# Optimization experiments

Measured on AMD Instinct MI355X. Metric: run time of the kernel, lower is better.

Reference implementation:

```python
import jax, jax.numpy as jnp
import numpy as np


def setup_inputs() -> dict:
    key = jax.random.key(0)
    ks = jax.random.split(key, 5)
    B, S, D = 2, 2048, 1024
    x = jax.random.normal(ks[0], (B, S, D), dtype=jnp.float32)
    # nn.Linear default init scale ~ 1/sqrt(fan_in); use scaled normals
    W_qkv = jax.random.normal(ks[1], (3 * D, D), dtype=jnp.float32) * (1.0 / np.sqrt(D))
    b_qkv = jax.random.normal(ks[2], (3 * D,), dtype=jnp.float32) * 0.01
    W_out = jax.random.normal(ks[3], (D, D), dtype=jnp.float32) * (1.0 / np.sqrt(D))
    b_out = jax.random.normal(ks[4], (D,), dtype=jnp.float32) * 0.01
    return {"x": x, "W_qkv": W_qkv, "b_qkv": b_qkv, "W_out": W_out, "b_out": b_out, "n_heads": 16}


def reference(x, W_qkv, b_qkv, W_out, b_out, n_heads):
    B, S, D = x.shape
    H = n_heads
    c = D // H
    scale = jnp.asarray(1.0 / np.sqrt(c), dtype=x.dtype)
    # qkv projection; torch layout: (head, qkv, c) along the 3*D output dim
    qkv = (x @ W_qkv.T + b_qkv).reshape(B, S, H, 3, c)
    q = qkv[..., 0, :]  # (B, S, H, c)
    k = qkv[..., 1, :]
    v = qkv[..., 2, :]
    scores = jnp.einsum("bshd,bthd->bhst", q, k) * scale  # (B, H, S, S)
    # mask='right': forbid attending to future positions (col > row)
    causal = jnp.arange(S)[None, :] > jnp.arange(S)[:, None]  # (S, S) True where future
    scores = jnp.where(causal[None, None], -jnp.inf, scores)
    attn = jax.nn.softmax(scores, axis=-1)
    ctx = jnp.einsum("bhst,bthd->bshd", attn, v).reshape(B, S, D)
    return ctx @ W_out.T + b_out
```

## Files before the change

### kernel.cpp

```cpp
#include <hip/hip_runtime.h>
#include <stdint.h>

#define B_ 2
#define S_ 2048
#define D_ 1024
#define H_ 16
#define C_ 64
#define M_ (B_*S_)
#define N1_ (3*D_)

typedef float f32x4 __attribute__((ext_vector_type(4)));
typedef float f32x16 __attribute__((ext_vector_type(16)));
typedef __bf16 bf16x8 __attribute__((ext_vector_type(8)));

#define QSCALE 0.18033688f

static __device__ __forceinline__ unsigned short f2bf(float f) {
  __bf16 h = (__bf16)f;
  return __builtin_bit_cast(unsigned short, h);
}
static __device__ __forceinline__ unsigned pk2(float lo, float hi) {
  return (unsigned)f2bf(lo) | ((unsigned)f2bf(hi) << 16);
}

static __device__ __forceinline__ f32x4 mfma_bf16(uint4 a, uint4 b, f32x4 c) {
  return __builtin_amdgcn_mfma_f32_16x16x32_bf16(
      __builtin_bit_cast(bf16x8, a), __builtin_bit_cast(bf16x8, b), c, 0, 0, 0);
}
static __device__ __forceinline__ f32x16 mfma32(uint4 a, uint4 b, f32x16 c) {
  return __builtin_amdgcn_mfma_f32_32x32x16_bf16(
      __builtin_bit_cast(bf16x8, a), __builtin_bit_cast(bf16x8, b), c, 0, 0, 0);
}

static __device__ __forceinline__ float xsum32(float x) {
  return x + __shfl_xor(x, 32);
}

static __device__ __forceinline__ void gload16(const void* g, void* l) {
  __builtin_amdgcn_global_load_lds(
      (const __attribute__((address_space(1))) unsigned int*)g,
      (__attribute__((address_space(3))) unsigned int*)l, 16, 0, 0);
}

#define N8X (M_*D_/8)
#define N8W (N1_*D_/8)
#define N8O (D_*D_/8)
__global__ __launch_bounds__(256) void cast_all(
    const float* __restrict__ x,   unsigned short* __restrict__ xb,
    const float* __restrict__ wq,  unsigned short* __restrict__ wqb,
    const float* __restrict__ wo,  unsigned short* __restrict__ wob) {
  int i = blockIdx.x * 256 + threadIdx.x;
  const float* src; unsigned short* dst; int j;
  if (i < N8X)              { src = x;  dst = xb;  j = i; }
  else if (i < N8X + N8W)   { src = wq; dst = wqb; j = i - N8X; }
  else                      { src = wo; dst = wob; j = i - N8X - N8W; }
  const float4* s4 = (const float4*)src;
  float4 a = s4[2*j], b = s4[2*j+1];
  uint4 o;
  o.x = pk2(a.x, a.y);
  o.y = pk2(a.z, a.w);
  o.z = pk2(b.x, b.y);
  o.w = pk2(b.z, b.w);
  ((uint4*)dst)[j] = o;
}

template<int MODE>
__global__ __launch_bounds__(256) void gemm_bt(
    const unsigned short* __restrict__ A,
    const unsigned short* __restrict__ Bm,
    const float* __restrict__ bias,
    float* __restrict__ Cf,
    unsigned short* __restrict__ Qg,
    unsigned short* __restrict__ Kf,
    unsigned short* __restrict__ Vf,
    int Ndim, int Kdim)
{
  __shared__ __attribute__((aligned(16))) unsigned short As[2][128*64];
  __shared__ __attribute__((aligned(16))) unsigned short Bs[2][128*64];
  const int tid = threadIdx.x;
  const int l = tid & 63, wid = tid >> 6;
  const int g = l >> 4, lr = l & 15;
  const int m0 = blockIdx.y * 128, n0 = blockIdx.x * 128;
  const int wr = (wid >> 1) * 64, wc = (wid & 1) * 64;

  f32x4 acc[4][4] = {};

  const int srow8 = l >> 3;
  const int schunk = (l & 7) ^ srow8;
  const unsigned short* Agl = A + (size_t)(m0 + wid*32 + srow8) * Kdim + schunk*8;
  const unsigned short* Bgl = Bm + (size_t)(n0 + wid*32 + srow8) * Kdim + schunk*8;
  const int doff = (wid*32)*64;
  const size_t rstep = (size_t)8 * Kdim;

#define GSTAGE(BI, K0) do {                                        \
    _Pragma("unroll")                                              \
    for (int i_ = 0; i_ < 4; ++i_) {                               \
      gload16(Agl + (K0) + i_*rstep, &As[BI][doff + i_*8*64]);     \
      gload16(Bgl + (K0) + i_*rstep, &Bs[BI][doff + i_*8*64]);     \
    }                                                              \
  } while (0)

  GSTAGE(0, 0);
  __syncthreads();

  int cur = 0;
  for (int k0 = 0; k0 < Kdim; k0 += 64) {
    if (k0 + 64 < Kdim) GSTAGE(cur ^ 1, k0 + 64);
    const unsigned short* Ab = As[cur];
    const unsigned short* Bb = Bs[cur];
#pragma unroll
    for (int kk = 0; kk < 2; ++kk) {
      const int c = kk*4 + g;
      uint4 af[4], bf[4];
#pragma unroll
      for (int mi = 0; mi < 4; ++mi)
        af[mi] = *(const uint4*)&Ab[(wr + mi*16 + lr)*64 + ((c ^ (lr & 7))*8)];
#pragma unroll
      for (int ni = 0; ni < 4; ++ni)
        bf[ni] = *(const uint4*)&Bb[(wc + ni*16 + lr)*64 + ((c ^ (lr & 7))*8)];
#pragma unroll
      for (int mi = 0; mi < 4; ++mi)
#pragma unroll
        for (int ni = 0; ni < 4; ++ni)
          acc[mi][ni] = mfma_bf16(af[mi], bf[ni], acc[mi][ni]);
    }
    __syncthreads();
    cur ^= 1;
  }
#undef GSTAGE

#pragma unroll
  for (int mi = 0; mi < 4; ++mi)
#pragma unroll
    for (int ni = 0; ni < 4; ++ni) {
      if (MODE == 0) {
#pragma unroll
        for (int r = 0; r < 4; ++r) {
          const int row = m0 + wr + mi*16 + g*4 + r;
          const int col = n0 + wc + ni*16 + lr;
          Cf[(size_t)row * Ndim + col] = acc[mi][ni][r] + bias[col];
        }
      } else {
        const int colbase = n0 + wc + ni*16;
        const int h     = colbase / 192;
        const int rem   = colbase % 192;
        const int which = rem >> 6;
        const int cb    = rem & 63;
        const float bv  = bias[colbase + lr];
        const int row0  = m0 + wr + mi*16 + g*4;
        const int b     = row0 >> 11, s0 = row0 & 2047;
        const size_t bh32 = (size_t)(b*H_ + h) * 32;
        if (which == 0) {
#pragma unroll
          for (int r = 0; r < 4; ++r) {
            const float v = (acc[mi][ni][r] + bv) * QSCALE;
            Qg[((size_t)(b*H_ + h)*S_ + (s0 + r))*C_ + cb + lr] = f2bf(v);
          }
        } else if (which == 1) {
          const int kc = cb >> 4, hi = lr >> 3, j = lr & 7;
          const int kvb = s0 >> 6, kq = s0 & 63;
          const int half = kq >> 5, qlb = kq & 31;
          const size_t base = (((bh32 + kvb)*2 + half)*4 + kc)*512 + hi*256 + j;
#pragma unroll
          for (int r = 0; r < 4; ++r)
            Kf[base + (size_t)(qlb + r)*8] = f2bf(acc[mi][ni][r] + bv);
        } else {
          const int d = cb + lr;
          const int dhalf = d >> 5, ql = d & 31;
          const int kvb = s0 >> 6, kq = s0 & 63;
          const int kc = kq >> 4, hi = (kq >> 3) & 1, j0 = kq & 7;
          const size_t base = (((bh32 + kvb)*2 + dhalf)*4 + kc)*512
                              + (hi*32 + ql)*8 + j0;
          ushort4 pk;
          pk.x = f2bf(acc[mi][ni][0] + bv);
          pk.y = f2bf(acc[mi][ni][1] + bv);
          pk.z = f2bf(acc[mi][ni][2] + bv);
          pk.w = f2bf(acc[mi][ni][3] + bv);
          *(ushort4*)(Vf + base) = pk;
        }
      }
    }
}

#define PS_ 72
__global__ __launch_bounds__(256) void attn_fwd(
    const unsigned short* __restrict__ Qg,
    const unsigned short* __restrict__ Kf,
    const unsigned short* __restrict__ Vf,
    unsigned short* __restrict__ ctx)
{
  __shared__ __attribute__((aligned(16))) unsigned short Ps[4][32*PS_];
  float* Cmb0 = (float*)&Ps[0][0];
  float* Cmb1 = Cmb0 + 2112;

  const int tid = threadIdx.x, l = tid & 63, w = tid >> 6;
  const int ql = l & 31, hi = l >> 5;
  const int bh = blockIdx.x;
  const int qt = 63 - (int)blockIdx.y;
  const int qw0 = qt * 32;
  const int qg = qw0 + ql;
  const size_t baseK = (size_t)bh * S_ * C_;

  uint4 qreg[4];
  {
    const unsigned short* qp = Qg + baseK + (size_t)qg * C_ + hi * 8;
#pragma unroll
    for (int kc = 0; kc < 4; ++kc) qreg[kc] = *(const uint4*)(qp + 16*kc);
  }

  f32x16 acc0 = {}, acc1 = {};
  float lsum = 0.f;

  const unsigned short* pK = Kf + (size_t)bh * (32*4096) + (size_t)l * 8;
  const unsigned short* pV = Vf + (size_t)bh * (32*4096) + (size_t)l * 8;
  unsigned short* Pw = Ps[w];

  const int n_t = (qt + 2) >> 1;
  for (int i = w; i < n_t; i += 4) {
    const int kv0 = i * 64;
    const size_t kb = (size_t)i * 4096;

    uint4 kf0[4], kf1[4];
#pragma unroll
    for (int kc = 0; kc < 4; ++kc) {
      kf0[kc] = *(const uint4*)(pK + kb + kc*512);
      kf1[kc] = *(const uint4*)(pK + kb + 2048 + kc*512);
    }
    f32x16 st0 = {}, st1 = {};
    __builtin_amdgcn_s_setprio(1);
#pragma unroll
    for (int kc = 0; kc < 4; ++kc) {
      st0 = mfma32(kf0[kc], qreg[kc], st0);
      st1 = mfma32(kf1[kc], qreg[kc], st1);
    }
    __builtin_amdgcn_s_setprio(0);

    uint4 vf0[4], vf1[4];
#pragma unroll
    for (int kc = 0; kc < 4; ++kc) {
      vf0[kc] = *(const uint4*)(pV + kb + kc*512);
      vf1[kc] = *(const uint4*)(pV + kb + 2048 + kc*512);
    }

    if (kv0 + 63 > qw0) {
#pragma unroll
      for (int r = 0; r < 16; ++r) {
        const int krow = (r & 3) + 8*(r >> 2) + 4*hi;
        if (kv0 + krow      > qg) st0[r] = -1e30f;
        if (kv0 + 32 + krow > qg) st1[r] = -1e30f;
      }
    }

    float ps[8];
#pragma unroll
    for (int j = 0; j < 8; ++j) {
      st0[2*j]   = exp2f(st0[2*j]);
      st0[2*j+1] = exp2f(st0[2*j+1]);
      st1[2*j]   = exp2f(st1[2*j]);
      st1[2*j+1] = exp2f(st1[2*j+1]);
      ps[j] = (st0[2*j] + st0[2*j+1]) + (st1[2*j] + st1[2*j+1]);
    }
    ps[0] += ps[4]; ps[1] += ps[5]; ps[2] += ps[6]; ps[3] += ps[7];
    lsum += (ps[0] + ps[1]) + (ps[2] + ps[3]);

#pragma unroll
    for (int r = 0; r < 16; r += 4) {
      const int k0i = (r >> 2)*8 + 4*hi;
      uint2 a0, a1;
      a0.x = pk2(st0[r],   st0[r+1]);  a0.y = pk2(st0[r+2], st0[r+3]);
      a1.x = pk2(st1[r],   st1[r+1]);  a1.y = pk2(st1[r+2], st1[r+3]);
      *(uint2*)&Pw[ql*PS_ + k0i]      = a0;
      *(uint2*)&Pw[ql*PS_ + 32 + k0i] = a1;
    }
    uint4 pb[4];
#pragma unroll
    for (int kc = 0; kc < 4; ++kc)
      pb[kc] = *(const uint4*)&Pw[ql*PS_ + kc*16 + hi*8];

    __builtin_amdgcn_s_setprio(1);
#pragma unroll
    for (int kc = 0; kc < 4; ++kc) {
      acc0 = mfma32(vf0[kc], pb[kc], acc0);
      acc1 = mfma32(vf1[kc], pb[kc], acc1);
    }
    __builtin_amdgcn_s_setprio(0);
  }

  __syncthreads();
  if (w >= 2) {
    float* Cb = (w == 2) ? Cmb0 : Cmb1;
#pragma unroll
    for (int r = 0; r < 16; ++r) {
      const int d0 = (r & 3) + 8*(r >> 2) + 4*hi;
      Cb[d0*32 + ql]        = acc0[r];
      Cb[(d0 + 32)*32 + ql] = acc1[r];
    }
    Cb[2048 + l] = lsum;
  }
  __syncthreads();
  if (w < 2) {
    const float* Cb = (w == 0) ? Cmb0 : Cmb1;
#pragma unroll
    for (int r = 0; r < 16; ++r) {
      const int d0 = (r & 3) + 8*(r >> 2) + 4*hi;
      acc0[r] += Cb[d0*32 + ql];
      acc1[r] += Cb[(d0 + 32)*32 + ql];
    }
    lsum += Cb[2048 + l];
  }
  __syncthreads();
  if (w == 1) {
    float* Cb = Cmb0;
#pragma unroll
    for (int r = 0; r < 16; ++r) {
      const int d0 = (r & 3) + 8*(r >> 2) + 4*hi;
      Cb[d0*32 + ql]        = acc0[r];
      Cb[(d0 + 32)*32 + ql] = acc1[r];
    }
    Cb[2048 + l] = lsum;
  }
  __syncthreads();
  if (w != 0) return;
  {
    const float* Cb = Cmb0;
#pragma unroll
    for (int r = 0; r < 16; ++r) {
      const int d0 = (r & 3) + 8*(r >> 2) + 4*hi;
      acc0[r] += Cb[d0*32 + ql];
      acc1[r] += Cb[(d0 + 32)*32 + ql];
    }
    lsum += Cb[2048 + l];
  }

  const float inv = 1.0f / xsum32(lsum);
#pragma unroll
  for (int r = 0; r < 16; ++r) {
    const int d0 = (r & 3) + 8*(r >> 2) + 4*hi;
    Pw[ql*PS_ + ( d0       ^ (8*(ql & 7)))] = f2bf(acc0[r] * inv);
    Pw[ql*PS_ + ((32 + d0) ^ (8*(ql & 7)))] = f2bf(acc1[r] * inv);
  }
  const int q1 = l >> 1, half = l & 1;
  const unsigned short* Er = Pw + q1*PS_;
  const int b = bh >> 4, h = bh & 15;
  unsigned short* outp = ctx + ((size_t)(b*S_ + qw0 + q1))*D_ + h*C_;
#pragma unroll
  for (int j = 0; j < 4; ++j) {
    const int clog = half*4 + j;
    const int cx = clog ^ (q1 & 7);
    uint4 val = *(const uint4*)&Er[cx*8];
    *(uint4*)(outp + clog*8) = val;
  }
}

extern "C" void kernel_launch(void* const* d_in, const int* in_sizes, int n_in,
                              void* d_out, int out_size, void* d_ws, size_t ws_size,
                              hipStream_t stream) {
  const float* x    = (const float*)d_in[0];
  const float* Wqkv = (const float*)d_in[1];
  const float* bqkv = (const float*)d_in[2];
  const float* Wout = (const float*)d_in[3];
  const float* bout = (const float*)d_in[4];
  float* out = (float*)d_out;

  unsigned short* ws = (unsigned short*)d_ws;
  unsigned short* xb    = ws;
  unsigned short* wqkvb = xb    + (size_t)M_ * D_;
  unsigned short* woutb = wqkvb + (size_t)N1_ * D_;
  unsigned short* Qb    = woutb + (size_t)D_ * D_;
  unsigned short* Kfb   = Qb    + (size_t)B_*H_*S_*C_;
  unsigned short* Vfb   = Kfb   + (size_t)B_*H_*S_*C_;
  unsigned short* ctxb  = Vfb   + (size_t)B_*H_*S_*C_;

  {
    const int ntot = N8X + N8W + N8O;
    cast_all<<<dim3((ntot+255)/256), dim3(256), 0, stream>>>(
        x, xb, Wqkv, wqkvb, Wout, woutb);
  }

  gemm_bt<1><<<dim3(N1_/128, M_/128), dim3(256), 0, stream>>>(
      xb, wqkvb, bqkv, nullptr, Qb, Kfb, Vfb, N1_, D_);

  attn_fwd<<<dim3(32, 64), dim3(256), 0, stream>>>(Qb, Kfb, Vfb, ctxb);

  gemm_bt<0><<<dim3(D_/128, M_/128), dim3(256), 0, stream>>>(
      ctxb, woutb, bout, out, nullptr, nullptr, nullptr, D_, D_);
}
```

Measured before the change: 118.5 us.

## Use eight waves per attention block and swizzle GEMM block order for XCDs

```diff
diff --git a/kernel.cpp b/kernel.cpp
--- a/kernel.cpp
+++ b/kernel.cpp
@@ -80,7 +80,11 @@
   const int tid = threadIdx.x;
   const int l = tid & 63, wid = tid >> 6;
   const int g = l >> 4, lr = l & 15;
-  const int m0 = blockIdx.y * 128, n0 = blockIdx.x * 128;
+  const int nbx = gridDim.x;
+  const int nwg = nbx * gridDim.y;
+  int lin = (int)blockIdx.x + nbx * (int)blockIdx.y;
+  lin = (lin & 7) * (nwg >> 3) + (lin >> 3);
+  const int m0 = (lin / nbx) * 128, n0 = (lin % nbx) * 128;
   const int wr = (wid >> 1) * 64, wc = (wid & 1) * 64;
 
   f32x4 acc[4][4] = {};
@@ -183,15 +187,14 @@
 }
 
 #define PS_ 72
-__global__ __launch_bounds__(256) void attn_fwd(
+__global__ __launch_bounds__(512) void attn_fwd(
     const unsigned short* __restrict__ Qg,
     const unsigned short* __restrict__ Kf,
     const unsigned short* __restrict__ Vf,
     unsigned short* __restrict__ ctx)
 {
-  __shared__ __attribute__((aligned(16))) unsigned short Ps[4][32*PS_];
-  float* Cmb0 = (float*)&Ps[0][0];
-  float* Cmb1 = Cmb0 + 2112;
+  __shared__ __attribute__((aligned(16))) unsigned short Ps[8][32*PS_];
+  float* CmbB = (float*)&Ps[0][0];
 
   const int tid = threadIdx.x, l = tid & 63, w = tid >> 6;
   const int ql = l & 31, hi = l >> 5;
@@ -216,7 +219,7 @@
   unsigned short* Pw = Ps[w];
 
   const int n_t = (qt + 2) >> 1;
-  for (int i = w; i < n_t; i += 4) {
+  for (int i = w; i < n_t; i += 8) {
     const int kv0 = i * 64;
     const size_t kb = (size_t)i * 4096;
 
@@ -286,51 +289,42 @@
     __builtin_amdgcn_s_setprio(0);
   }
 
-  __syncthreads();
-  if (w >= 2) {
-    float* Cb = (w == 2) ? Cmb0 : Cmb1;
-#pragma unroll
-    for (int r = 0; r < 16; ++r) {
-      const int d0 = (r & 3) + 8*(r >> 2) + 4*hi;
-      Cb[d0*32 + ql]        = acc0[r];
-      Cb[(d0 + 32)*32 + ql] = acc1[r];
-    }
-    Cb[2048 + l] = lsum;
-  }
-  __syncthreads();
-  if (w < 2) {
-    const float* Cb = (w == 0) ? Cmb0 : Cmb1;
-#pragma unroll
-    for (int r = 0; r < 16; ++r) {
-      const int d0 = (r & 3) + 8*(r >> 2) + 4*hi;
-      acc0[r] += Cb[d0*32 + ql];
-      acc1[r] += Cb[(d0 + 32)*32 + ql];
-    }
-    lsum += Cb[2048 + l];
-  }
-  __syncthreads();
-  if (w == 1) {
-    float* Cb = Cmb0;
-#pragma unroll
-    for (int r = 0; r < 16; ++r) {
-      const int d0 = (r & 3) + 8*(r >> 2) + 4*hi;
-      Cb[d0*32 + ql]        = acc0[r];
-      Cb[(d0 + 32)*32 + ql] = acc1[r];
-    }
-    Cb[2048 + l] = lsum;
-  }
+#define PUBLISH(REG) do {                                          \
+    float* Cb_ = CmbB + (REG)*2112;                                \
+    _Pragma("unroll")                                              \
+    for (int r = 0; r < 16; ++r) {                                 \
+      const int d0_ = (r & 3) + 8*(r >> 2) + 4*hi;                 \
+      Cb_[d0_*32 + ql]        = acc0[r];                           \
+      Cb_[(d0_ + 32)*32 + ql] = acc1[r];                           \
+    }                                                              \
+    Cb_[2048 + l] = lsum;                                          \
+  } while (0)
+#define ABSORB(REG) do {                                           \
+    const float* Cb_ = CmbB + (REG)*2112;                          \
+    _Pragma("unroll")                                              \
+    for (int r = 0; r < 16; ++r) {                                 \
+      const int d0_ = (r & 3) + 8*(r >> 2) + 4*hi;                 \
+      acc0[r] += Cb_[d0_*32 + ql];                                 \
+      acc1[r] += Cb_[(d0_ + 32)*32 + ql];                          \
+    }                                                              \
+    lsum += Cb_[2048 + l];                                         \
+  } while (0)
+
+  __syncthreads();
+  if (w >= 4) PUBLISH(w - 4);
+  __syncthreads();
+  if (w < 4) ABSORB(w);
+  __syncthreads();
+  if (w == 2 || w == 3) PUBLISH(w - 2);
+  __syncthreads();
+  if (w < 2) ABSORB(w);
+  __syncthreads();
+  if (w == 1) PUBLISH(0);
   __syncthreads();
   if (w != 0) return;
-  {
-    const float* Cb = Cmb0;
-#pragma unroll
-    for (int r = 0; r < 16; ++r) {
-      const int d0 = (r & 3) + 8*(r >> 2) + 4*hi;
-      acc0[r] += Cb[d0*32 + ql];
-      acc1[r] += Cb[(d0 + 32)*32 + ql];
-    }
-    lsum += Cb[2048 + l];
-  }
+  ABSORB(0);
+#undef PUBLISH
+#undef ABSORB
 
   const float inv = 1.0f / xsum32(lsum);
 #pragma unroll
@@ -380,7 +374,7 @@
   gemm_bt<1><<<dim3(N1_/128, M_/128), dim3(256), 0, stream>>>(
       xb, wqkvb, bqkv, nullptr, Qb, Kfb, Vfb, N1_, D_);
 
-  attn_fwd<<<dim3(32, 64), dim3(256), 0, stream>>>(Qb, Kfb, Vfb, ctxb);
+  attn_fwd<<<dim3(32, 64), dim3(512), 0, stream>>>(Qb, Kfb, Vfb, ctxb);
 
   gemm_bt<0><<<dim3(D_/128, M_/128), dim3(256), 0, stream>>>(
       ctxb, woutb, bout, out, nullptr, nullptr, nullptr, D_, D_);
```

New measurement: 129.5 us. +9.3%, slower.

## Pair light and heavy causal query tiles per attention block

Applied to the files above, without the earlier changes.

```diff
diff --git a/kernel.cpp b/kernel.cpp
--- a/kernel.cpp
+++ b/kernel.cpp
@@ -196,7 +196,10 @@
   const int tid = threadIdx.x, l = tid & 63, w = tid >> 6;
   const int ql = l & 31, hi = l >> 5;
   const int bh = blockIdx.x;
-  const int qt = 63 - (int)blockIdx.y;
+  const int y = (int)blockIdx.y;
+  const int pairi = w >> 1;
+  const int ws = w & 1;
+  const int qt = pairi ? (63 - y) : y;
   const int qw0 = qt * 32;
   const int qg = qw0 + ql;
   const size_t baseK = (size_t)bh * S_ * C_;
@@ -216,7 +219,7 @@
   unsigned short* Pw = Ps[w];
 
   const int n_t = (qt + 2) >> 1;
-  for (int i = w; i < n_t; i += 4) {
+  for (int i = ws; i < n_t; i += 2) {
     const int kv0 = i * 64;
     const size_t kb = (size_t)i * 4096;
 
@@ -287,8 +290,8 @@
   }
 
   __syncthreads();
-  if (w >= 2) {
-    float* Cb = (w == 2) ? Cmb0 : Cmb1;
+  if (ws == 1) {
+    float* Cb = (w == 1) ? Cmb0 : Cmb1;
 #pragma unroll
     for (int r = 0; r < 16; ++r) {
       const int d0 = (r & 3) + 8*(r >> 2) + 4*hi;
@@ -298,31 +301,9 @@
     Cb[2048 + l] = lsum;
   }
   __syncthreads();
-  if (w < 2) {
+  if (ws != 0) return;
+  {
     const float* Cb = (w == 0) ? Cmb0 : Cmb1;
-#pragma unroll
-    for (int r = 0; r < 16; ++r) {
-      const int d0 = (r & 3) + 8*(r >> 2) + 4*hi;
-      acc0[r] += Cb[d0*32 + ql];
-      acc1[r] += Cb[(d0 + 32)*32 + ql];
-    }
-    lsum += Cb[2048 + l];
-  }
-  __syncthreads();
-  if (w == 1) {
-    float* Cb = Cmb0;
-#pragma unroll
-    for (int r = 0; r < 16; ++r) {
-      const int d0 = (r & 3) + 8*(r >> 2) + 4*hi;
-      Cb[d0*32 + ql]        = acc0[r];
-      Cb[(d0 + 32)*32 + ql] = acc1[r];
-    }
-    Cb[2048 + l] = lsum;
-  }
-  __syncthreads();
-  if (w != 0) return;
-  {
-    const float* Cb = Cmb0;
 #pragma unroll
     for (int r = 0; r < 16; ++r) {
       const int d0 = (r & 3) + 8*(r >> 2) + 4*hi;
@@ -380,7 +361,7 @@
   gemm_bt<1><<<dim3(N1_/128, M_/128), dim3(256), 0, stream>>>(
       xb, wqkvb, bqkv, nullptr, Qb, Kfb, Vfb, N1_, D_);
 
-  attn_fwd<<<dim3(32, 64), dim3(256), 0, stream>>>(Qb, Kfb, Vfb, ctxb);
+  attn_fwd<<<dim3(32, 32), dim3(256), 0, stream>>>(Qb, Kfb, Vfb, ctxb);
 
   gemm_bt<0><<<dim3(D_/128, M_/128), dim3(256), 0, stream>>>(
       ctxb, woutb, bout, out, nullptr, nullptr, nullptr, D_, D_);
```

After: 126.2 us. +6.5%, slower.
